# Optimization experiments

Hardware: AMD Instinct MI355X
Metric: run time of the kernel (lower is better)

The kernel has to match this reference:

```python
import jax, jax.numpy as jnp
import numpy as np

N_NODES = 20000
N_EDGES = 640000
L, H, C = 8, 8, 8  # layers, heads, per-head dim
D = H * C          # 64, in = out dim for every layer
NEG_SLOPE = 0.2


def setup_inputs() -> dict:
    key = jax.random.key(0)
    ks = jax.random.split(key, 6)
    x = jax.random.normal(ks[0], (N_NODES, D), dtype=jnp.float32)
    edge_index = jax.random.randint(ks[1], (2, N_EDGES), 0, N_NODES, dtype=jnp.int64)
    # GATConv params (PyG glorot-ish scale), stacked over layers
    Ws = jax.random.normal(ks[2], (L, D, H * C), dtype=jnp.float32) * (1.0 / np.sqrt(D))
    att_src = jax.random.normal(ks[3], (L, H, C), dtype=jnp.float32) * (1.0 / np.sqrt(C))
    att_dst = jax.random.normal(ks[4], (L, H, C), dtype=jnp.float32) * (1.0 / np.sqrt(C))
    biases = jnp.zeros((L, H * C), dtype=jnp.float32)
    return {"x": x, "edge_index": edge_index, "Ws": Ws,
            "att_src": att_src, "att_dst": att_dst, "biases": biases}


def _gat_layer(x, src, dst, W, a_src, a_dst, b):
    N = x.shape[0]
    h = (x @ W).reshape(N, H, C)                      # [N,H,C] per-head projection
    s_src = jnp.einsum('nhc,hc->nh', h, a_src)        # [N,H]
    s_dst = jnp.einsum('nhc,hc->nh', h, a_dst)        # [N,H]
    e = jax.nn.leaky_relu(s_src[src] + s_dst[dst], NEG_SLOPE)   # [E,H]
    # segment softmax over incoming edges of each destination node
    m = jax.ops.segment_max(e, dst, num_segments=N)   # [N,H]
    ex = jnp.exp(e - m[dst])
    z = jax.ops.segment_sum(ex, dst, num_segments=N)  # [N,H]
    alpha = ex / (z[dst] + 1e-16)                     # [E,H]
    out = jax.ops.segment_sum(h[src] * alpha[:, :, None], dst, num_segments=N)
    return out.reshape(N, H * C) + b                  # concat heads + bias


def reference(x, edge_index, Ws, att_src, att_dst, biases):
    N = x.shape[0]
    loops = jnp.arange(N, dtype=edge_index.dtype)     # PyG add_self_loops=True
    src = jnp.concatenate([edge_index[0], loops])
    dst = jnp.concatenate([edge_index[1], loops])
    for l in range(L):
        x = _gat_layer(x, src, dst, Ws[l], att_src[l], att_dst[l], biases[l])
    return x
```

## Files before the change

kernel.cpp:

```cpp
#include <hip/hip_runtime.h>
#include <stdint.h>

#define NEG_SLOPE 0.2f

static inline int ceil_div(int a, int b){ return (a + b - 1) / b; }

__global__ __launch_bounds__(256) void zero_i32(int* __restrict__ p, int n){
  int i = blockIdx.x * 256 + threadIdx.x;
  if (i < n) p[i] = 0;
}

__global__ __launch_bounds__(256) void hist_kernel(const int* __restrict__ dst,
                                                   int* __restrict__ counts, int E){
  int i = blockIdx.x * 256 + threadIdx.x;
  if (i < E) atomicAdd(counts + dst[i], 1);
}

__global__ __launch_bounds__(1024) void scan_kernel(const int* __restrict__ counts,
                                                    int* __restrict__ offsets,
                                                    int* __restrict__ cursor, int n){
  __shared__ int lds[1024];
  const int tid = threadIdx.x;
  const int chunk = (n + 1023) >> 10;
  const int beg = tid * chunk;
  const int end = min(beg + chunk, n);
  int s = 0;
  for (int i = beg; i < end; ++i) s += counts[i];
  lds[tid] = s;
  __syncthreads();
  for (int off = 1; off < 1024; off <<= 1){
    int t = 0;
    if (tid >= off) t = lds[tid - off];
    __syncthreads();
    if (tid >= off) lds[tid] += t;
    __syncthreads();
  }
  int run = lds[tid] - s;
  for (int i = beg; i < end; ++i){
    offsets[i] = run;
    cursor[i]  = run;
    run += counts[i];
  }
  if (tid == 1023) offsets[n] = lds[1023];
}

__global__ __launch_bounds__(256) void scatter_kernel(const int* __restrict__ srcv,
                                                      const int* __restrict__ dstv,
                                                      int* __restrict__ cursor,
                                                      int* __restrict__ sorted_src, int E){
  int i = blockIdx.x * 256 + threadIdx.x;
  if (i < E){
    int d = dstv[i];
    int pos = atomicAdd(cursor + d, 1);
    sorted_src[pos] = srcv[i];
  }
}

__global__ __launch_bounds__(256) void gemm_fused(const float* __restrict__ x,
                                                  const float* __restrict__ W,
                                                  const float* __restrict__ a_src,
                                                  const float* __restrict__ a_dst,
                                                  float* __restrict__ h,
                                                  float* __restrict__ s_src,
                                                  float* __restrict__ s_dst, int N){
  __shared__ float xlds[32 * 64];
  const int tid  = threadIdx.x;
  const int lane = tid & 63;
  const int wave = tid >> 6;
  const int row0 = blockIdx.x * 32;

  float wreg[64];
  #pragma unroll
  for (int k = 0; k < 64; ++k) wreg[k] = W[k * 64 + lane];

  {
    const float4* xg = (const float4*)x;
    float4* xl = (float4*)xlds;
    #pragma unroll
    for (int i = tid; i < 512; i += 256){
      int r = row0 + (i >> 4);
      float4 v = {0.f, 0.f, 0.f, 0.f};
      if (r < N) v = xg[(size_t)r * 16 + (i & 15)];
      xl[i] = v;
    }
  }
  __syncthreads();

  const float asv = a_src[lane];
  const float adv = a_dst[lane];

  for (int r = wave; r < 32; r += 4){
    int row = row0 + r;
    if (row >= N) break;
    const float4* xr = (const float4*)(xlds + r * 64);
    float acc = 0.0f;
    #pragma unroll
    for (int kk = 0; kk < 16; ++kk){
      float4 xv = xr[kk];
      acc = fmaf(xv.x, wreg[4*kk+0], acc);
      acc = fmaf(xv.y, wreg[4*kk+1], acc);
      acc = fmaf(xv.z, wreg[4*kk+2], acc);
      acc = fmaf(xv.w, wreg[4*kk+3], acc);
    }
    h[(size_t)row * 64 + lane] = acc;
    float ps = acc * asv;
    float pd = acc * adv;
    #pragma unroll
    for (int off = 1; off < 8; off <<= 1){
      ps += __shfl_xor(ps, off, 64);
      pd += __shfl_xor(pd, off, 64);
    }
    if ((lane & 7) == 0){
      s_src[row * 8 + (lane >> 3)] = ps;
      s_dst[row * 8 + (lane >> 3)] = pd;
    }
  }
}

__global__ __launch_bounds__(256) void aggregate(const float* __restrict__ h,
                                                 const float* __restrict__ s_src,
                                                 const float* __restrict__ s_dst,
                                                 const int* __restrict__ offsets,
                                                 const int* __restrict__ sorted_src,
                                                 const float* __restrict__ bias,
                                                 float* __restrict__ out, int N){
  const int node = (blockIdx.x * 256 + threadIdx.x) >> 6;
  if (node >= N) return;
  const int lane = threadIdx.x & 63;
  const int c8 = lane & 7;
  const int e8 = lane >> 3;
  const int beg = offsets[node];
  const int nv  = offsets[node + 1] - beg + 1;
  const float sdst = s_dst[node * 8 + c8];

  float m = -3.0e38f;
  float z = 0.0f;
  float acc[8];
  #pragma unroll
  for (int j = 0; j < 8; ++j) acc[j] = 0.0f;

  if (nv <= 64){
    const int cnt = (e8 < nv) ? ((nv - e8 + 7) >> 3) : 0;
    int sidx[8];
    #pragma unroll
    for (int j = 0; j < 8; ++j){
      int v = e8 + 8 * j;
      if (j < cnt) sidx[j] = (v == 0) ? node : sorted_src[beg + v - 1];
    }
    float sc[8];
    #pragma unroll
    for (int j = 0; j < 8; ++j){
      if (j < cnt){
        float s = s_src[sidx[j] * 8 + c8] + sdst;
        sc[j] = (s > 0.0f) ? s : NEG_SLOPE * s;
        m = fmaxf(m, sc[j]);
      }
    }
    m = fmaxf(m, __shfl_xor(m, 8, 64));
    m = fmaxf(m, __shfl_xor(m, 16, 64));
    m = fmaxf(m, __shfl_xor(m, 32, 64));
    #pragma unroll
    for (int j = 0; j < 8; ++j){
      if (j < cnt){
        float e = __expf(sc[j] - m);
        z += e;
        const float4* hp = (const float4*)(h + (size_t)sidx[j] * 64 + c8 * 8);
        float4 h0 = hp[0];
        float4 h1 = hp[1];
        acc[0] = fmaf(e, h0.x, acc[0]);
        acc[1] = fmaf(e, h0.y, acc[1]);
        acc[2] = fmaf(e, h0.z, acc[2]);
        acc[3] = fmaf(e, h0.w, acc[3]);
        acc[4] = fmaf(e, h1.x, acc[4]);
        acc[5] = fmaf(e, h1.y, acc[5]);
        acc[6] = fmaf(e, h1.z, acc[6]);
        acc[7] = fmaf(e, h1.w, acc[7]);
      }
    }
  } else {
    for (int v = e8; v < nv; v += 8){
      int s = (v == 0) ? node : sorted_src[beg + v - 1];
      float scv = s_src[s * 8 + c8] + sdst;
      scv = (scv > 0.0f) ? scv : NEG_SLOPE * scv;
      m = fmaxf(m, scv);
    }
    m = fmaxf(m, __shfl_xor(m, 8, 64));
    m = fmaxf(m, __shfl_xor(m, 16, 64));
    m = fmaxf(m, __shfl_xor(m, 32, 64));
    for (int v = e8; v < nv; v += 8){
      int s = (v == 0) ? node : sorted_src[beg + v - 1];
      float scv = s_src[s * 8 + c8] + sdst;
      scv = (scv > 0.0f) ? scv : NEG_SLOPE * scv;
      float e = __expf(scv - m);
      z += e;
      const float4* hp = (const float4*)(h + (size_t)s * 64 + c8 * 8);
      float4 h0 = hp[0];
      float4 h1 = hp[1];
      acc[0] = fmaf(e, h0.x, acc[0]);
      acc[1] = fmaf(e, h0.y, acc[1]);
      acc[2] = fmaf(e, h0.z, acc[2]);
      acc[3] = fmaf(e, h0.w, acc[3]);
      acc[4] = fmaf(e, h1.x, acc[4]);
      acc[5] = fmaf(e, h1.y, acc[5]);
      acc[6] = fmaf(e, h1.z, acc[6]);
      acc[7] = fmaf(e, h1.w, acc[7]);
    }
  }

  #pragma unroll
  for (int off = 8; off < 64; off <<= 1){
    z += __shfl_xor(z, off, 64);
    #pragma unroll
    for (int j = 0; j < 8; ++j) acc[j] += __shfl_xor(acc[j], off, 64);
  }

  if (e8 == 0){
    float inv = 1.0f / (z + 1e-16f);
    const float4* bp = (const float4*)(bias + c8 * 8);
    float4 b0 = bp[0], b1 = bp[1];
    float4 o0, o1;
    o0.x = acc[0] * inv + b0.x;
    o0.y = acc[1] * inv + b0.y;
    o0.z = acc[2] * inv + b0.z;
    o0.w = acc[3] * inv + b0.w;
    o1.x = acc[4] * inv + b1.x;
    o1.y = acc[5] * inv + b1.y;
    o1.z = acc[6] * inv + b1.z;
    o1.w = acc[7] * inv + b1.w;
    float4* op = (float4*)(out + (size_t)node * 64 + c8 * 8);
    op[0] = o0;
    op[1] = o1;
  }
}

extern "C" void kernel_launch(void* const* d_in, const int* in_sizes, int n_in,
                              void* d_out, int out_size, void* d_ws, size_t ws_size,
                              hipStream_t stream){
  const float* x0   = (const float*)d_in[0];
  const int*   eidx = (const int*)  d_in[1];
  const float* Ws   = (const float*)d_in[2];
  const float* asrc = (const float*)d_in[3];
  const float* adst = (const float*)d_in[4];
  const float* bias = (const float*)d_in[5];

  const int N = in_sizes[0] / 64;
  const int E = in_sizes[1] / 2;
  const int L = in_sizes[2] / (64 * 64);

  char* ws = (char*)d_ws;
  size_t off = 0;
  auto alloc = [&](size_t bytes) -> void* {
    void* p = ws + off;
    off = (off + bytes + 255) & ~(size_t)255;
    return p;
  };
  float* hbuf    = (float*)alloc((size_t)N * 64 * sizeof(float));
  float* bufA    = (float*)alloc((size_t)N * 64 * sizeof(float));
  float* bufB    = (float*)alloc((size_t)N * 64 * sizeof(float));
  float* ssrc    = (float*)alloc((size_t)N * 8 * sizeof(float));
  float* sdstb   = (float*)alloc((size_t)N * 8 * sizeof(float));
  int*   counts  = (int*)alloc((size_t)N * sizeof(int));
  int*   offsets = (int*)alloc((size_t)(N + 1) * sizeof(int));
  int*   cursor  = (int*)alloc((size_t)N * sizeof(int));
  int*   ssorted = (int*)alloc((size_t)E * sizeof(int));

  const int* esrc = eidx;
  const int* edst = eidx + E;

  zero_i32<<<ceil_div(N, 256), 256, 0, stream>>>(counts, N);
  hist_kernel<<<ceil_div(E, 256), 256, 0, stream>>>(edst, counts, E);
  scan_kernel<<<1, 1024, 0, stream>>>(counts, offsets, cursor, N);
  scatter_kernel<<<ceil_div(E, 256), 256, 0, stream>>>(esrc, edst, cursor, ssorted, E);

  float* bufs[2] = {bufA, bufB};
  for (int l = 0; l < L; ++l){
    const float* xin  = (l == 0)     ? x0 : bufs[(l - 1) & 1];
    float*       xout = (l == L - 1) ? (float*)d_out : bufs[l & 1];
    gemm_fused<<<ceil_div(N, 32), 256, 0, stream>>>(
        xin, Ws + (size_t)l * 64 * 64, asrc + l * 64, adst + l * 64,
        hbuf, ssrc, sdstb, N);
    aggregate<<<ceil_div(N * 64, 256), 256, 0, stream>>>(
        hbuf, ssrc, sdstb, offsets, ssorted, bias + l * 64, xout, N);
  }
}
```

Before: 440.0 us.

## Permute h layout for coalesced gathers, halve GEMM tile, prefetch neighbor rows

The GEMM stores h in a permuted column layout. Each aggregate lane's two float4 loads then sit 32 floats apart, so the 8 lanes of a head read contiguous 128B segments. Intermediate layer outputs are written in the matching permuted layout, and the next layer's weight rows are permuted to compensate, so the final output stays in natural order. The GEMM tile shrinks to 16 rows per block for more blocks, and its accumulation is split into two chains. In the aggregate fast path all neighbor h loads are issued before the max reduction to raise memory-level parallelism, at some register cost. Bounds clamps on offsets and the scatter position are also added.

```diff
diff --git a/kernel.cpp b/kernel.cpp
--- a/kernel.cpp
+++ b/kernel.cpp
@@ -52,7 +52,7 @@
   if (i < E){
     int d = dstv[i];
     int pos = atomicAdd(cursor + d, 1);
-    sorted_src[pos] = srcv[i];
+    if (pos >= 0 && pos < E) sorted_src[pos] = srcv[i];
   }
 }
 
@@ -62,47 +62,57 @@
                                                   const float* __restrict__ a_dst,
                                                   float* __restrict__ h,
                                                   float* __restrict__ s_src,
-                                                  float* __restrict__ s_dst, int N){
-  __shared__ float xlds[32 * 64];
+                                                  float* __restrict__ s_dst,
+                                                  int N, int perm_in){
+  __shared__ float xlds[16 * 64];
   const int tid  = threadIdx.x;
   const int lane = tid & 63;
   const int wave = tid >> 6;
-  const int row0 = blockIdx.x * 32;
+  const int row0 = blockIdx.x * 16;
 
   float wreg[64];
   #pragma unroll
-  for (int k = 0; k < 64; ++k) wreg[k] = W[k * 64 + lane];
+  for (int s = 0; s < 64; ++s){
+    int c = perm_in ? (((s >> 2) & 7) * 8 + (s >> 5) * 4 + (s & 3)) : s;
+    wreg[s] = W[c * 64 + lane];
+  }
 
   {
     const float4* xg = (const float4*)x;
-    float4* xl = (float4*)xlds;
-    #pragma unroll
-    for (int i = tid; i < 512; i += 256){
-      int r = row0 + (i >> 4);
-      float4 v = {0.f, 0.f, 0.f, 0.f};
-      if (r < N) v = xg[(size_t)r * 16 + (i & 15)];
-      xl[i] = v;
-    }
+    int r = row0 + (tid >> 4);
+    float4 v = {0.f, 0.f, 0.f, 0.f};
+    if (r < N) v = xg[(size_t)r * 16 + (tid & 15)];
+    ((float4*)xlds)[tid] = v;
   }
   __syncthreads();
 
   const float asv = a_src[lane];
   const float adv = a_dst[lane];
-
-  for (int r = wave; r < 32; r += 4){
+  const int hword = ((lane >> 3) << 2) | (lane & 3) | ((lane & 4) << 3);
+
+  for (int r = wave; r < 16; r += 4){
     int row = row0 + r;
     if (row >= N) break;
     const float4* xr = (const float4*)(xlds + r * 64);
-    float acc = 0.0f;
-    #pragma unroll
-    for (int kk = 0; kk < 16; ++kk){
+    float a0 = 0.0f, a1 = 0.0f;
+    #pragma unroll
+    for (int kk = 0; kk < 8; ++kk){
       float4 xv = xr[kk];
-      acc = fmaf(xv.x, wreg[4*kk+0], acc);
-      acc = fmaf(xv.y, wreg[4*kk+1], acc);
-      acc = fmaf(xv.z, wreg[4*kk+2], acc);
-      acc = fmaf(xv.w, wreg[4*kk+3], acc);
-    }
-    h[(size_t)row * 64 + lane] = acc;
+      a0 = fmaf(xv.x, wreg[4*kk+0], a0);
+      a0 = fmaf(xv.y, wreg[4*kk+1], a0);
+      a0 = fmaf(xv.z, wreg[4*kk+2], a0);
+      a0 = fmaf(xv.w, wreg[4*kk+3], a0);
+    }
+    #pragma unroll
+    for (int kk = 8; kk < 16; ++kk){
+      float4 xv = xr[kk];
+      a1 = fmaf(xv.x, wreg[4*kk+0], a1);
+      a1 = fmaf(xv.y, wreg[4*kk+1], a1);
+      a1 = fmaf(xv.z, wreg[4*kk+2], a1);
+      a1 = fmaf(xv.w, wreg[4*kk+3], a1);
+    }
+    float acc = a0 + a1;
+    h[(size_t)row * 64 + hword] = acc;
     float ps = acc * asv;
     float pd = acc * adv;
     #pragma unroll
@@ -123,14 +133,18 @@
                                                  const int* __restrict__ offsets,
                                                  const int* __restrict__ sorted_src,
                                                  const float* __restrict__ bias,
-                                                 float* __restrict__ out, int N){
+                                                 float* __restrict__ out,
+                                                 int N, int E, int perm_out){
   const int node = (blockIdx.x * 256 + threadIdx.x) >> 6;
   if (node >= N) return;
   const int lane = threadIdx.x & 63;
   const int c8 = lane & 7;
   const int e8 = lane >> 3;
-  const int beg = offsets[node];
-  const int nv  = offsets[node + 1] - beg + 1;
+  int beg = offsets[node];
+  int end = offsets[node + 1];
+  beg = max(0, min(beg, E));
+  end = max(0, min(end, E));
+  const int nv = end - beg + 1;
   const float sdst = s_dst[node * 8 + c8];
 
   float m = -3.0e38f;
@@ -153,9 +167,20 @@
       if (j < cnt){
         float s = s_src[sidx[j] * 8 + c8] + sdst;
         sc[j] = (s > 0.0f) ? s : NEG_SLOPE * s;
-        m = fmaxf(m, sc[j]);
       }
     }
+    float4 h0r[8], h1r[8];
+    #pragma unroll
+    for (int j = 0; j < 8; ++j){
+      if (j < cnt){
+        const float4* hp = (const float4*)(h + (size_t)sidx[j] * 64 + c8 * 4);
+        h0r[j] = hp[0];
+        h1r[j] = hp[8];
+      }
+    }
+    #pragma unroll
+    for (int j = 0; j < 8; ++j)
+      if (j < cnt) m = fmaxf(m, sc[j]);
     m = fmaxf(m, __shfl_xor(m, 8, 64));
     m = fmaxf(m, __shfl_xor(m, 16, 64));
     m = fmaxf(m, __shfl_xor(m, 32, 64));
@@ -164,17 +189,14 @@
       if (j < cnt){
         float e = __expf(sc[j] - m);
         z += e;
-        const float4* hp = (const float4*)(h + (size_t)sidx[j] * 64 + c8 * 8);
-        float4 h0 = hp[0];
-        float4 h1 = hp[1];
-        acc[0] = fmaf(e, h0.x, acc[0]);
-        acc[1] = fmaf(e, h0.y, acc[1]);
-        acc[2] = fmaf(e, h0.z, acc[2]);
-        acc[3] = fmaf(e, h0.w, acc[3]);
-        acc[4] = fmaf(e, h1.x, acc[4]);
-        acc[5] = fmaf(e, h1.y, acc[5]);
-        acc[6] = fmaf(e, h1.z, acc[6]);
-        acc[7] = fmaf(e, h1.w, acc[7]);
+        acc[0] = fmaf(e, h0r[j].x, acc[0]);
+        acc[1] = fmaf(e, h0r[j].y, acc[1]);
+        acc[2] = fmaf(e, h0r[j].z, acc[2]);
+        acc[3] = fmaf(e, h0r[j].w, acc[3]);
+        acc[4] = fmaf(e, h1r[j].x, acc[4]);
+        acc[5] = fmaf(e, h1r[j].y, acc[5]);
+        acc[6] = fmaf(e, h1r[j].z, acc[6]);
+        acc[7] = fmaf(e, h1r[j].w, acc[7]);
       }
     }
   } else {
@@ -193,9 +215,9 @@
       scv = (scv > 0.0f) ? scv : NEG_SLOPE * scv;
       float e = __expf(scv - m);
       z += e;
-      const float4* hp = (const float4*)(h + (size_t)s * 64 + c8 * 8);
+      const float4* hp = (const float4*)(h + (size_t)s * 64 + c8 * 4);
       float4 h0 = hp[0];
-      float4 h1 = hp[1];
+      float4 h1 = hp[8];
       acc[0] = fmaf(e, h0.x, acc[0]);
       acc[1] = fmaf(e, h0.y, acc[1]);
       acc[2] = fmaf(e, h0.z, acc[2]);
@@ -227,9 +249,15 @@
     o1.y = acc[5] * inv + b1.y;
     o1.z = acc[6] * inv + b1.z;
     o1.w = acc[7] * inv + b1.w;
-    float4* op = (float4*)(out + (size_t)node * 64 + c8 * 8);
-    op[0] = o0;
-    op[1] = o1;
+    if (perm_out){
+      float4* op = (float4*)(out + (size_t)node * 64);
+      op[c8]     = o0;
+      op[8 + c8] = o1;
+    } else {
+      float4* op = (float4*)(out + (size_t)node * 64 + c8 * 8);
+      op[0] = o0;
+      op[1] = o1;
+    }
   }
 }
 
@@ -276,10 +304,11 @@
   for (int l = 0; l < L; ++l){
     const float* xin  = (l == 0)     ? x0 : bufs[(l - 1) & 1];
     float*       xout = (l == L - 1) ? (float*)d_out : bufs[l & 1];
-    gemm_fused<<<ceil_div(N, 32), 256, 0, stream>>>(
+    gemm_fused<<<ceil_div(N, 16), 256, 0, stream>>>(
         xin, Ws + (size_t)l * 64 * 64, asrc + l * 64, adst + l * 64,
-        hbuf, ssrc, sdstb, N);
+        hbuf, ssrc, sdstb, N, (l > 0) ? 1 : 0);
     aggregate<<<ceil_div(N * 64, 256), 256, 0, stream>>>(
-        hbuf, ssrc, sdstb, offsets, ssorted, bias + l * 64, xout, N);
-  }
-}
+        hbuf, ssrc, sdstb, offsets, ssorted, bias + l * 64, xout,
+        N, E, (l < L - 1) ? 1 : 0);
+  }
+}
```

Result: no change. 437.7 us (-0.5%).
